# Optimization experiments

Measured on AMD Instinct MI355X. Metric: run time of the kernel, lower is better.

## Reference

```python
import jax, jax.numpy as jnp
import numpy as np

C = 128  # hidden_dim


def setup_inputs() -> dict:
    key = jax.random.key(0)
    ks = jax.random.split(key, 8)
    B, H, W = 4, 64, 64
    x1 = jax.random.normal(ks[0], (B, C, H, W), dtype=jnp.float32)
    x2 = jax.random.normal(ks[1], (B, C, H, W), dtype=jnp.float32)
    # 1x1 conv == per-pixel linear over channels; store weights as [C_out, C_in]
    s = 1.0 / np.sqrt(C)
    wq = jax.random.uniform(ks[2], (C, C), jnp.float32, -s, s)
    bq = jax.random.uniform(ks[3], (C,), jnp.float32, -s, s)
    wk = jax.random.uniform(ks[4], (C, C), jnp.float32, -s, s)
    bk = jax.random.uniform(ks[5], (C,), jnp.float32, -s, s)
    wv = jax.random.uniform(ks[6], (C, C), jnp.float32, -s, s)
    bv = jax.random.uniform(ks[7], (C,), jnp.float32, -s, s)
    return {"x1": x1, "x2": x2, "wq": wq, "bq": bq, "wk": wk, "bk": bk, "wv": wv, "bv": bv}


def reference(x1, x2, wq, bq, wk, bk, wv, bv):
    B, Cc, H, W = x1.shape
    N = H * W
    # flatten spatial -> tokens: [B, N, C]
    t1 = x1.reshape(B, Cc, N).transpose(0, 2, 1)
    t2 = x2.reshape(B, Cc, N).transpose(0, 2, 1)
    # 1x1 conv projections (per-token linear)
    q = jnp.einsum('bnc,oc->bno', t1, wq) + bq
    k = jnp.einsum('bnc,oc->bno', t2, wk) + bk
    v = jnp.einsum('bnc,oc->bno', t2, wv) + bv
    scale = 1.0 / jnp.sqrt(jnp.asarray(Cc, x1.dtype))
    attn = jax.nn.softmax(jnp.einsum('bqc,bkc->bqk', q, k) * scale, axis=-1)
    out = jnp.einsum('bqk,bkc->bqc', attn, v)  # [B, N, C]
    out = out.transpose(0, 2, 1).reshape(B, Cc, H, W)
    return out + x1
```

## Files before the change

kernel.cpp:

```cpp
#include <hip/hip_runtime.h>
#include <hip/hip_bf16.h>

typedef float  f32x4  __attribute__((ext_vector_type(4)));
typedef float  f32x16 __attribute__((ext_vector_type(16)));
typedef short  s16x8  __attribute__((ext_vector_type(8)));
typedef int    i32x8  __attribute__((ext_vector_type(8)));
typedef unsigned int   u32x2 __attribute__((ext_vector_type(2)));
typedef unsigned int   u32x4 __attribute__((ext_vector_type(4)));

#define B_ 4
#define C_ 128
#define N_ 4096
#define NST 16
#define QSCALE 0.12751744f

__device__ __forceinline__ unsigned int pkbf(float lo, float hi) {
    union { float f; unsigned int u; } a, b; a.f = lo; b.f = hi;
    return __builtin_amdgcn_perm(b.u + 0x8000u, a.u + 0x8000u, 0x07060302u);
}
__device__ __forceinline__ unsigned int pk_fp8x4(float a, float b, float c, float d) {
    int v = __builtin_amdgcn_cvt_pk_fp8_f32(a, b, 0, false);
    v = __builtin_amdgcn_cvt_pk_fp8_f32(c, d, v, true);
    return (unsigned int)v;
}
__device__ __forceinline__ s16x8 mk_frag(unsigned int a, unsigned int b,
                                         unsigned int c, unsigned int d) {
    union { u32x4 u; s16x8 v; } t; t.u = (u32x4){a, b, c, d}; return t.v;
}
__device__ __forceinline__ f32x16 z16() {
    f32x16 v;
    #pragma unroll
    for (int r = 0; r < 16; r++) v[r] = 0.f;
    return v;
}
__device__ __forceinline__ i32x8 ld32g(const unsigned char* p) {
    union { u32x4 q[2]; i32x8 v; } t;
    t.q[0] = *(const u32x4*)p;
    t.q[1] = *(const u32x4*)(p + 1024);
    return t.v;
}
__device__ __forceinline__ f32x16 mfs(i32x8 a, i32x8 b, f32x16 c) {
    return __builtin_amdgcn_mfma_scale_f32_32x32x64_f8f6f4(
        a, b, c, 0, 0, 0, 0x7F7F7F7Fu, 0, 0x7F7F7F7Fu);
}

__global__ __launch_bounds__(256) void wcvt_kernel(
    const float* __restrict__ wq, const float* __restrict__ wk,
    const float* __restrict__ wv, unsigned short* __restrict__ Wf)
{
    const int gid = blockIdx.x * 256 + threadIdx.x;
    const int l = gid & 63, fid = gid >> 6;
    const int kc = fid & 7, ot = (fid >> 3) & 3, z = fid >> 5;
    const float* w = (z == 0) ? wq : (z == 1 ? wk : wv);
    const int o  = 32 * ot + (l & 31);
    const int c0 = 16 * kc + 8 * (l >> 5);
    const float* src = &w[o * C_ + c0];
    *(u32x4*)&Wf[fid * 512 + l * 8] = (u32x4){
        pkbf(src[0], src[1]), pkbf(src[2], src[3]),
        pkbf(src[4], src[5]), pkbf(src[6], src[7])};
}

__global__ __launch_bounds__(256, 2) void proj_kernel(
    const float* __restrict__ x1, const float* __restrict__ x2,
    const float* __restrict__ bq, const float* __restrict__ bk,
    const float* __restrict__ bv,
    const unsigned short* __restrict__ Wf,
    unsigned char* __restrict__ Qf, unsigned char* __restrict__ Kf,
    unsigned char* __restrict__ Vf)
{
    __shared__ float Xs[2][C_ * 36];
    const int tid = threadIdx.x;
    const int ot  = tid >> 6;
    const int l = tid & 63, lo = l & 31, h = l >> 5;
    const int bid = blockIdx.x;
    const int b = bid & 3, tb = bid >> 2;
    const int n0 = tb * 32;

    {
        const int q = tid & 7, c0 = tid >> 3;
        #pragma unroll
        for (int cc = 0; cc < 4; cc++) {
            const int c = c0 + 32 * cc;
            const size_t gof = ((size_t)b * C_ + c) * N_ + n0 + 4 * q;
            *(f32x4*)&Xs[0][c * 36 + 4 * q] = *(const f32x4*)&x1[gof];
            *(f32x4*)&Xs[1][c * 36 + 4 * q] = *(const f32x4*)&x2[gof];
        }
    }
    __syncthreads();

    auto ldW = [&](int z, int kc) -> s16x8 {
        return *(const s16x8*)&Wf[(((z * 4 + ot) * 8) + kc) * 512 + l * 8];
    };
    auto xfrag = [&](int z, int kc) -> s16x8 {
        const float* p = &Xs[z][(16 * kc + 8 * h) * 36 + lo];
        float f[8];
        #pragma unroll
        for (int i = 0; i < 8; i++) f[i] = p[i * 36];
        return mk_frag(pkbf(f[0], f[1]), pkbf(f[2], f[3]),
                       pkbf(f[4], f[5]), pkbf(f[6], f[7]));
    };

    f32x16 aq = z16(), ak = z16(), av = z16();
    s16x8 wqA = ldW(0, 0), wkA = ldW(1, 0), wvA = ldW(2, 0);
    s16x8 wqB, wkB, wvB;
    #pragma unroll
    for (int kc = 0; kc < 8; kc++) {
        if (kc & 1) {
            if (kc < 7) { wqA = ldW(0, kc + 1); wkA = ldW(1, kc + 1); wvA = ldW(2, kc + 1); }
            s16x8 f1 = xfrag(0, kc), f2 = xfrag(1, kc);
            aq = __builtin_amdgcn_mfma_f32_32x32x16_bf16(wqB, f1, aq, 0, 0, 0);
            ak = __builtin_amdgcn_mfma_f32_32x32x16_bf16(wkB, f2, ak, 0, 0, 0);
            av = __builtin_amdgcn_mfma_f32_32x32x16_bf16(f2, wvB, av, 0, 0, 0);
        } else {
            if (kc < 7) { wqB = ldW(0, kc + 1); wkB = ldW(1, kc + 1); wvB = ldW(2, kc + 1); }
            s16x8 f1 = xfrag(0, kc), f2 = xfrag(1, kc);
            aq = __builtin_amdgcn_mfma_f32_32x32x16_bf16(wqA, f1, aq, 0, 0, 0);
            ak = __builtin_amdgcn_mfma_f32_32x32x16_bf16(wkA, f2, ak, 0, 0, 0);
            av = __builtin_amdgcn_mfma_f32_32x32x16_bf16(f2, wvA, av, 0, 0, 0);
        }
    }

    const size_t fbase = (size_t)(b * 128 + tb) * 4096;
    #pragma unroll
    for (int rq = 0; rq < 4; rq++) {
        const int o0 = 32 * ot + 8 * rq + 4 * h;
        const f32x4 b4q = *(const f32x4*)&bq[o0];
        const f32x4 b4k = *(const f32x4*)&bk[o0];
        const size_t off = fbase + (ot >> 1) * 2048 + (rq >> 1) * 1024
                         + ((ot & 1) * 32 + lo) * 16 + 8 * (rq & 1) + 4 * h;
        *(unsigned int*)&Qf[off] = pk_fp8x4(
            (aq[4*rq+0] + b4q[0]) * QSCALE, (aq[4*rq+1] + b4q[1]) * QSCALE,
            (aq[4*rq+2] + b4q[2]) * QSCALE, (aq[4*rq+3] + b4q[3]) * QSCALE);
        *(unsigned int*)&Kf[off] = pk_fp8x4(
            ak[4*rq+0] + b4k[0], ak[4*rq+1] + b4k[1],
            ak[4*rq+2] + b4k[2], ak[4*rq+3] + b4k[3]);
    }
    {
        const float bvv = bv[32 * ot + lo];
        const size_t vbase = ((size_t)(b * 64 + (tb >> 1)) * 4 + ot) * 2048;
        #pragma unroll
        for (int rq = 0; rq < 4; rq++) {
            const size_t off = vbase + (rq >> 1) * 1024
                             + ((tb & 1) * 32 + lo) * 16 + 8 * (rq & 1) + 4 * h;
            *(unsigned int*)&Vf[off] = pk_fp8x4(
                av[4*rq+0] + bvv, av[4*rq+1] + bvv,
                av[4*rq+2] + bvv, av[4*rq+3] + bvv);
        }
    }
}

__global__ __launch_bounds__(512, 2) void attn_kernel(
    const unsigned char* __restrict__ Qf,
    const unsigned char* __restrict__ Kf,
    const unsigned char* __restrict__ Vf,
    const float* __restrict__ x1,
    float* __restrict__ out)
{
    __shared__ float Ol[4 * 128 * 33];
    __shared__ float Llds[8][32];

    const int tid = threadIdx.x;
    const int w  = tid >> 6;
    const int qi = w & 1, ps = w >> 1;
    const int l = tid & 63, lo = l & 31, h = l >> 5;
    const int bid = blockIdx.x;
    const int xcd = bid & 7, slot = bid >> 3;
    const int b  = xcd >> 1;
    const int qt = ((xcd & 1) << 5) | slot;
    const int q0 = qt * 64;

    const unsigned char* Kb = Kf + (size_t)b * 524288 + 2 * ps * 4096 + l * 16;
    const unsigned char* Vb = Vf + (size_t)b * 524288 + ps * 8192 + l * 16;

    i32x8 qb0, qb1;
    {
        const unsigned char* qp = Qf + (size_t)(b * 128 + qt * 2 + qi) * 4096 + l * 16;
        qb0 = ld32g(qp);
        qb1 = ld32g(qp + 2048);
    }

    f32x16 oacc[4];
    #pragma unroll
    for (int ct = 0; ct < 4; ct++) oacc[ct] = z16();
    float La = 0.f, Lb2 = 0.f;

    i32x8 k0, k1, k2, k3;
    {
        const unsigned char* Kg = Kb + (size_t)(slot & 15) * 32768;
        k0 = ld32g(Kg);        k1 = ld32g(Kg + 2048);
        k2 = ld32g(Kg + 4096); k3 = ld32g(Kg + 6144);
    }

    #pragma unroll
    for (int t = 0; t < NST; t++) {
        const int tp = (t + slot) & 15;
        const unsigned char* Vg = Vb + (size_t)tp * 32768;
        i32x8 v0 = ld32g(Vg);        i32x8 v1 = ld32g(Vg + 2048);
        i32x8 v2 = ld32g(Vg + 4096); i32x8 v3 = ld32g(Vg + 6144);
        i32x8 n0, n1, n2, n3;
        if (t + 1 < NST) {
            const unsigned char* Kg = Kb + (size_t)((t + 1 + slot) & 15) * 32768;
            n0 = ld32g(Kg);        n1 = ld32g(Kg + 2048);
            n2 = ld32g(Kg + 4096); n3 = ld32g(Kg + 6144);
        }
        f32x16 s0 = z16(), s1 = z16();
        s0 = mfs(k0, qb0, s0);
        s0 = mfs(k1, qb1, s0);
        s1 = mfs(k2, qb0, s1);
        s1 = mfs(k3, qb1, s1);
        float e0[16], e1[16];
        #pragma unroll
        for (int r = 0; r < 16; r++) {
            e0[r] = __builtin_amdgcn_exp2f(s0[r]);
            e1[r] = __builtin_amdgcn_exp2f(s1[r]);
        }
        #pragma unroll
        for (int r = 0; r < 8; r++) { La += e0[r] + e1[r]; Lb2 += e0[r+8] + e1[r+8]; }
        union { unsigned int u[8]; i32x8 v; } pb;
        #pragma unroll
        for (int j = 0; j < 4; j++) {
            const unsigned int w0 = pk_fp8x4(e0[4*j], e0[4*j+1], e0[4*j+2], e0[4*j+3]);
            const unsigned int w1 = pk_fp8x4(e1[4*j], e1[4*j+1], e1[4*j+2], e1[4*j+3]);
            u32x2 sw = __builtin_amdgcn_permlane32_swap(w0, w1, false, false);
            pb.u[2*j]   = sw[0];
            pb.u[2*j+1] = sw[1];
        }
        const i32x8 pB = pb.v;
        oacc[0] = mfs(v0, pB, oacc[0]);
        oacc[1] = mfs(v1, pB, oacc[1]);
        oacc[2] = mfs(v2, pB, oacc[2]);
        oacc[3] = mfs(v3, pB, oacc[3]);
        k0 = n0; k1 = n1; k2 = n2; k3 = n3;
    }

    const float Lh = La + Lb2;
    const float Lsum = Lh + __shfl_xor(Lh, 32, 64);
    if (l < 32) Llds[w][lo] = Lsum;
    __syncthreads();

    for (int g = 0; g < 2; g++) {
        if (qi == g) {
            #pragma unroll
            for (int ct = 0; ct < 4; ct++)
                #pragma unroll
                for (int r = 0; r < 16; r++) {
                    const int c = 32 * ct + (r & 3) + 8 * (r >> 2) + 4 * h;
                    Ol[ps * 4224 + c * 33 + lo] = oacc[ct][r];
                }
        }
        __syncthreads();
        {
            const int c = tid >> 2, qq = tid & 3;
            const size_t gbase = ((size_t)b * C_ + c) * N_ + q0 + g * 32 + qq * 8;
            float v[8];
            #pragma unroll
            for (int j = 0; j < 8; j++) {
                const int q = qq * 8 + j;
                const float ssum = Ol[c * 33 + q]        + Ol[4224  + c * 33 + q]
                                 + Ol[8448 + c * 33 + q] + Ol[12672 + c * 33 + q];
                const float Lq = Llds[g][q] + Llds[2 + g][q]
                               + Llds[4 + g][q] + Llds[6 + g][q];
                v[j] = ssum * __builtin_amdgcn_rcpf(Lq);
            }
            const f32x4 xlo = *(const f32x4*)&x1[gbase];
            const f32x4 xhi = *(const f32x4*)&x1[gbase + 4];
            *(f32x4*)&out[gbase]     = (f32x4){v[0]+xlo[0], v[1]+xlo[1], v[2]+xlo[2], v[3]+xlo[3]};
            *(f32x4*)&out[gbase + 4] = (f32x4){v[4]+xhi[0], v[5]+xhi[1], v[6]+xhi[2], v[7]+xhi[3]};
        }
        __syncthreads();
    }
}

extern "C" void kernel_launch(void* const* d_in, const int* in_sizes, int n_in,
                              void* d_out, int out_size, void* d_ws, size_t ws_size,
                              hipStream_t stream)
{
    const float* x1 = (const float*)d_in[0];
    const float* x2 = (const float*)d_in[1];
    const float* wq = (const float*)d_in[2];
    const float* bq = (const float*)d_in[3];
    const float* wk = (const float*)d_in[4];
    const float* bk = (const float*)d_in[5];
    const float* wv = (const float*)d_in[6];
    const float* bv = (const float*)d_in[7];
    float* out = (float*)d_out;

    unsigned short* Wf = (unsigned short*)d_ws;
    unsigned char* Qf = (unsigned char*)d_ws + 98304;
    unsigned char* Kf = Qf + (size_t)B_ * 128 * 4096;
    unsigned char* Vf = Kf + (size_t)B_ * 128 * 4096;

    wcvt_kernel<<<24, 256, 0, stream>>>(wq, wk, wv, Wf);
    proj_kernel<<<512, 256, 0, stream>>>(x1, x2, bq, bk, bv, Wf, Qf, Kf, Vf);
    attn_kernel<<<256, 512, 0, stream>>>(Qf, Kf, Vf, x1, out);
}
```

Measured before the change: 42.52 us.

## Stage K/V tiles through LDS with async global_load_lds and wave-pair flag sync

Each pair of waves sharing a key partition now cooperatively copies K and V tiles into a double-buffered LDS region using global_load_lds. One wave loads the K half and the other the V half, and the two signal each other through LDS flags with spin-waits instead of block barriers. This halves redundant global loads per wave pair and overlaps the next tile's fetch with compute. In exchange it adds 128KB of LDS use, which may limit occupancy below the two blocks per CU the launch bounds request, plus spin-wait overhead and a loop that is no longer fully unrolled.

```diff
diff --git a/kernel.cpp b/kernel.cpp
--- a/kernel.cpp
+++ b/kernel.cpp
@@ -14,6 +14,9 @@
 #define NST 16
 #define QSCALE 0.12751744f
 
+typedef __attribute__((address_space(3))) unsigned int       lds_u32;
+typedef __attribute__((address_space(1))) const unsigned int glb_u32;
+
 __device__ __forceinline__ unsigned int pkbf(float lo, float hi) {
     union { float f; unsigned int u; } a, b; a.f = lo; b.f = hi;
     return __builtin_amdgcn_perm(b.u + 0x8000u, a.u + 0x8000u, 0x07060302u);
@@ -42,6 +45,9 @@
 __device__ __forceinline__ f32x16 mfs(i32x8 a, i32x8 b, f32x16 c) {
     return __builtin_amdgcn_mfma_scale_f32_32x32x64_f8f6f4(
         a, b, c, 0, 0, 0, 0x7F7F7F7Fu, 0, 0x7F7F7F7Fu);
+}
+__device__ __forceinline__ void cp16(const unsigned char* g, unsigned char* l) {
+    __builtin_amdgcn_global_load_lds((glb_u32*)g, (lds_u32*)l, 16, 0, 0);
 }
 
 __global__ __launch_bounds__(256) void wcvt_kernel(
@@ -156,7 +162,8 @@
     const float* __restrict__ x1,
     float* __restrict__ out)
 {
-    __shared__ float Ol[4 * 128 * 33];
+    __shared__ __align__(16) unsigned char smem[131072];
+    __shared__ int flg[4][2][2];
     __shared__ float Llds[8][32];
 
     const int tid = threadIdx.x;
@@ -169,8 +176,11 @@
     const int qt = ((xcd & 1) << 5) | slot;
     const int q0 = qt * 64;
 
-    const unsigned char* Kb = Kf + (size_t)b * 524288 + 2 * ps * 4096 + l * 16;
+    const unsigned char* Kb = Kf + (size_t)b * 524288 + ps * 8192 + l * 16;
     const unsigned char* Vb = Vf + (size_t)b * 524288 + ps * 8192 + l * 16;
+    const size_t lbase = (size_t)ps * 32768;
+
+    if (tid < 16) ((int*)flg)[tid] = -1;
 
     i32x8 qb0, qb1;
     {
@@ -178,36 +188,53 @@
         qb0 = ld32g(qp);
         qb1 = ld32g(qp + 2048);
     }
+    __syncthreads();
+
+    volatile int* mySp = &flg[ps][0][qi];
+    volatile int* paSp = &flg[ps][0][qi ^ 1];
+    volatile int* myRp = &flg[ps][1][qi];
+    volatile int* paRp = &flg[ps][1][qi ^ 1];
+
+    auto stage_half = [&](int t) {
+        unsigned char* db = smem + lbase + (size_t)(t & 1) * 16384 + (qi ? 8192 : 0);
+        const unsigned char* src = (qi ? Vb : Kb) + (size_t)((t + slot) & 15) * 32768;
+        #pragma unroll
+        for (int j = 0; j < 8; j++) cp16(src + j * 1024, db + j * 1024);
+    };
+    auto lfrag = [&](size_t off) -> i32x8 {
+        union { u32x4 q[2]; i32x8 v; } t;
+        t.q[0] = *(const u32x4*)&smem[off];
+        t.q[1] = *(const u32x4*)&smem[off + 1024];
+        return t.v;
+    };
 
     f32x16 oacc[4];
     #pragma unroll
     for (int ct = 0; ct < 4; ct++) oacc[ct] = z16();
     float La = 0.f, Lb2 = 0.f;
 
-    i32x8 k0, k1, k2, k3;
-    {
-        const unsigned char* Kg = Kb + (size_t)(slot & 15) * 32768;
-        k0 = ld32g(Kg);        k1 = ld32g(Kg + 2048);
-        k2 = ld32g(Kg + 4096); k3 = ld32g(Kg + 6144);
-    }
-
-    #pragma unroll
+    stage_half(0);
+    stage_half(1);
+    asm volatile("s_waitcnt vmcnt(8)" ::: "memory");
+    if (l == 0) *mySp = 0;
+
     for (int t = 0; t < NST; t++) {
-        const int tp = (t + slot) & 15;
-        const unsigned char* Vg = Vb + (size_t)tp * 32768;
-        i32x8 v0 = ld32g(Vg);        i32x8 v1 = ld32g(Vg + 2048);
-        i32x8 v2 = ld32g(Vg + 4096); i32x8 v3 = ld32g(Vg + 6144);
-        i32x8 n0, n1, n2, n3;
-        if (t + 1 < NST) {
-            const unsigned char* Kg = Kb + (size_t)((t + 1 + slot) & 15) * 32768;
-            n0 = ld32g(Kg);        n1 = ld32g(Kg + 2048);
-            n2 = ld32g(Kg + 4096); n3 = ld32g(Kg + 6144);
-        }
+        while (*paSp < t) __builtin_amdgcn_s_sleep(1);
+        __builtin_amdgcn_sched_barrier(0);
+        const size_t sb = lbase + (size_t)(t & 1) * 16384 + (size_t)l * 16;
+        i32x8 k0 = lfrag(sb);
+        i32x8 k1 = lfrag(sb + 2048);
+        i32x8 k2 = lfrag(sb + 4096);
+        i32x8 k3 = lfrag(sb + 6144);
         f32x16 s0 = z16(), s1 = z16();
         s0 = mfs(k0, qb0, s0);
         s0 = mfs(k1, qb1, s0);
         s1 = mfs(k2, qb0, s1);
         s1 = mfs(k3, qb1, s1);
+        i32x8 v0 = lfrag(sb + 8192);
+        i32x8 v1 = lfrag(sb + 10240);
+        i32x8 v2 = lfrag(sb + 12288);
+        i32x8 v3 = lfrag(sb + 14336);
         float e0[16], e1[16];
         #pragma unroll
         for (int r = 0; r < 16; r++) {
@@ -216,21 +243,33 @@
         }
         #pragma unroll
         for (int r = 0; r < 8; r++) { La += e0[r] + e1[r]; Lb2 += e0[r+8] + e1[r+8]; }
-        union { unsigned int u[8]; i32x8 v; } pb;
+        union { unsigned int u[8]; i32x8 v; } pbu;
         #pragma unroll
         for (int j = 0; j < 4; j++) {
             const unsigned int w0 = pk_fp8x4(e0[4*j], e0[4*j+1], e0[4*j+2], e0[4*j+3]);
             const unsigned int w1 = pk_fp8x4(e1[4*j], e1[4*j+1], e1[4*j+2], e1[4*j+3]);
             u32x2 sw = __builtin_amdgcn_permlane32_swap(w0, w1, false, false);
-            pb.u[2*j]   = sw[0];
-            pb.u[2*j+1] = sw[1];
-        }
-        const i32x8 pB = pb.v;
-        oacc[0] = mfs(v0, pB, oacc[0]);
-        oacc[1] = mfs(v1, pB, oacc[1]);
-        oacc[2] = mfs(v2, pB, oacc[2]);
-        oacc[3] = mfs(v3, pB, oacc[3]);
-        k0 = n0; k1 = n1; k2 = n2; k3 = n3;
+            pbu.u[2*j]   = sw[0];
+            pbu.u[2*j+1] = sw[1];
+        }
+        const i32x8 pb = pbu.v;
+        oacc[0] = mfs(v0, pb, oacc[0]);
+        oacc[1] = mfs(v1, pb, oacc[1]);
+        oacc[2] = mfs(v2, pb, oacc[2]);
+        oacc[3] = mfs(v3, pb, oacc[3]);
+        asm volatile("s_waitcnt lgkmcnt(0)" ::: "memory");
+        __builtin_amdgcn_sched_barrier(0);
+        if (l == 0) *myRp = t;
+        if (t + 2 < NST) {
+            while (*paRp < t) __builtin_amdgcn_s_sleep(1);
+            __builtin_amdgcn_sched_barrier(0);
+            stage_half(t + 2);
+            asm volatile("s_waitcnt vmcnt(8)" ::: "memory");
+            if (l == 0) *mySp = t + 1;
+        } else if (t + 2 == NST) {
+            asm volatile("s_waitcnt vmcnt(0)" ::: "memory");
+            if (l == 0) *mySp = t + 1;
+        }
     }
 
     const float Lh = La + Lb2;
@@ -238,6 +277,7 @@
     if (l < 32) Llds[w][lo] = Lsum;
     __syncthreads();
 
+    float* Ol = (float*)smem;
     for (int g = 0; g < 2; g++) {
         if (qi == g) {
             #pragma unroll
```

New measurement: 45.54 us. 7.1% more time.
